# Kernel tuning notes

Measured on AMD Instinct MI355X. Metric: run time of the kernel, lower is better.

The kernel has to match this reference:

```python
import jax, jax.numpy as jnp
import numpy as np


def setup_inputs() -> dict:
    key = jax.random.key(0)
    ks = jax.random.split(key, 8)
    B, H, W = 4, 512, 256
    return {
        "x1": jax.random.normal(ks[0], (B, H, W), dtype=jnp.float32),
        "x2": jax.random.normal(ks[1], (B, H, W), dtype=jnp.float32),
        "wq": jax.random.normal(ks[2], (2, 2), dtype=jnp.float32) * 0.5,
        "bq": jax.random.normal(ks[3], (2,), dtype=jnp.float32) * 0.1,
        "wk": jax.random.normal(ks[4], (2, 2), dtype=jnp.float32) * 0.5,
        "bk": jax.random.normal(ks[5], (2,), dtype=jnp.float32) * 0.1,
        "wv": jax.random.normal(ks[6], (2, 2), dtype=jnp.float32) * 0.5,
        "bv": jax.random.normal(ks[7], (2,), dtype=jnp.float32) * 0.1,
    }


def reference(x1, x2, wq, bq, wk, bk, wv, bv):
    # input: [B, 2, H, W]
    inp = jnp.stack((x1, x2), axis=1)

    def proj(w, b):  # 1x1 conv == channel matmul; -> [B, 2, H, W]
        return jnp.einsum('oi,bihw->bohw', w, inp) + b[None, :, None, None]

    q = proj(wq, bq).transpose(0, 2, 3, 1)  # [B, H, W, 2]
    k = proj(wk, bk).transpose(0, 2, 1, 3)  # [B, H, 2, W]
    v = proj(wv, bv).transpose(0, 2, 3, 1)  # [B, H, W, 2]

    qk = jnp.einsum('bhwc,bhcu->bhwu', q, k)  # [B, H, W, W]
    score = jax.nn.softmax(qk, axis=-1)
    out = jnp.einsum('bhwu,bhuc->bhwc', score, v)  # [B, H, W, 2]

    out1 = x1 + out[..., 0]
    out2 = x2 + out[..., 1]
    return (out1, out2)
```

## Files before the change

kernel.cpp:

```cpp
#include <hip/hip_runtime.h>

typedef float v2f __attribute__((ext_vector_type(2)));

#define LOG2E 1.4426950408889634f

__device__ __forceinline__ float fast_exp2(float x) {
#if __has_builtin(__builtin_amdgcn_exp2f)
    return __builtin_amdgcn_exp2f(x);
#else
    return exp2f(x);
#endif
}

__device__ __forceinline__ v2f pk_fma(v2f a, v2f b, v2f c) {
    return __builtin_elementwise_fma(a, b, c);
}

__global__ __launch_bounds__(256, 2) void csa_kernel(
    const float* __restrict__ x1, const float* __restrict__ x2,
    const float* __restrict__ wq, const float* __restrict__ bq,
    const float* __restrict__ wk, const float* __restrict__ bk,
    const float* __restrict__ wv, const float* __restrict__ bv,
    float* __restrict__ out1, float* __restrict__ out2)
{
    constexpr int W = 256;
    __shared__ float4 sK[4][W / 2];
    __shared__ float4 sV[4][W / 2];

    const int tid = threadIdx.x;
    const int wv_id = tid >> 6;
    const int l = tid & 63;
    const long row = (long)blockIdx.x * 4 + wv_id;
    const long base = row * W;

    const float4 xa = *(const float4*)(x1 + base + 4 * l);
    const float4 xb = *(const float4*)(x2 + base + 4 * l);
    const float X1[4] = {xa.x, xa.y, xa.z, xa.w};
    const float X2[4] = {xb.x, xb.y, xb.z, xb.w};

    const float wq00 = wq[0], wq01 = wq[1], wq10 = wq[2], wq11 = wq[3];
    const float wk00 = wk[0], wk01 = wk[1], wk10 = wk[2], wk11 = wk[3];
    const float wv00 = wv[0], wv01 = wv[1], wv10 = wv[2], wv11 = wv[3];
    const float bq0 = bq[0], bq1 = bq[1];
    const float bk0 = bk[0], bk1 = bk[1];
    const float bv0 = bv[0], bv1 = bv[1];

    float q0[4], q1[4], k0[4], k1[4], v0[4], v1[4];
#pragma unroll
    for (int j = 0; j < 4; ++j) {
        q0[j] = fmaf(wq00, X1[j], fmaf(wq01, X2[j], bq0));
        q1[j] = fmaf(wq10, X1[j], fmaf(wq11, X2[j], bq1));
        k0[j] = fmaf(wk00, X1[j], fmaf(wk01, X2[j], bk0));
        k1[j] = fmaf(wk10, X1[j], fmaf(wk11, X2[j], bk1));
        v0[j] = fmaf(wv00, X1[j], fmaf(wv01, X2[j], bv0));
        v1[j] = fmaf(wv10, X1[j], fmaf(wv11, X2[j], bv1));
    }

    sK[wv_id][2 * l + 0] = make_float4(k0[0], k0[1], k1[0], k1[1]);
    sK[wv_id][2 * l + 1] = make_float4(k0[2], k0[3], k1[2], k1[3]);
    sV[wv_id][2 * l + 0] = make_float4(v0[0], v0[1], v1[0], v1[1]);
    sV[wv_id][2 * l + 1] = make_float4(v0[2], v0[3], v1[2], v1[3]);

    float q2 = 0.f, k2 = 0.f;
#pragma unroll
    for (int j = 0; j < 4; ++j) {
        q2 = fmaxf(q2, fmaf(q0[j], q0[j], q1[j] * q1[j]));
        k2 = fmaxf(k2, fmaf(k0[j], k0[j], k1[j] * k1[j]));
    }
#pragma unroll
    for (int off = 32; off >= 1; off >>= 1) {
        q2 = fmaxf(q2, __shfl_xor(q2, off, 64));
        k2 = fmaxf(k2, __shfl_xor(k2, off, 64));
    }
    const float mb = sqrtf(q2 * k2);
    const float csh = -mb * LOG2E;

    __syncthreads();

    const v2f cshv = {csh, csh};
    v2f ql0[4], ql1[4], sum[4], o0[4], o1[4];
#pragma unroll
    for (int j = 0; j < 4; ++j) {
        const float a0 = q0[j] * LOG2E, a1 = q1[j] * LOG2E;
        ql0[j] = (v2f){a0, a0};
        ql1[j] = (v2f){a1, a1};
        sum[j] = (v2f){0.f, 0.f};
        o0[j]  = (v2f){0.f, 0.f};
        o1[j]  = (v2f){0.f, 0.f};
    }

#pragma unroll 4
    for (int up = 0; up < W / 2; ++up) {
        const float4 K = sK[wv_id][up];
        const float4 V = sV[wv_id][up];
        const v2f kx = {K.x, K.y};
        const v2f kz = {K.z, K.w};
        const v2f vx = {V.x, V.y};
        const v2f vz = {V.z, V.w};
#pragma unroll
        for (int j = 0; j < 4; ++j) {
            v2f s = pk_fma(ql0[j], kx, pk_fma(ql1[j], kz, cshv));
            v2f e;
            e.x = fast_exp2(s.x);
            e.y = fast_exp2(s.y);
            sum[j] += e;
            o0[j] = pk_fma(e, vx, o0[j]);
            o1[j] = pk_fma(e, vz, o1[j]);
        }
    }

    float r1[4], r2[4];
#pragma unroll
    for (int j = 0; j < 4; ++j) {
        const float s = sum[j].x + sum[j].y;
        const float inv = 1.0f / s;
        r1[j] = fmaf(o0[j].x + o0[j].y, inv, X1[j]);
        r2[j] = fmaf(o1[j].x + o1[j].y, inv, X2[j]);
    }
    *(float4*)(out1 + base + 4 * l) = make_float4(r1[0], r1[1], r1[2], r1[3]);
    *(float4*)(out2 + base + 4 * l) = make_float4(r2[0], r2[1], r2[2], r2[3]);
}

extern "C" void kernel_launch(void* const* d_in, const int* in_sizes, int n_in,
                              void* d_out, int out_size, void* d_ws, size_t ws_size,
                              hipStream_t stream) {
    const float* x1 = (const float*)d_in[0];
    const float* x2 = (const float*)d_in[1];
    const float* wq = (const float*)d_in[2];
    const float* bq = (const float*)d_in[3];
    const float* wk = (const float*)d_in[4];
    const float* bk = (const float*)d_in[5];
    const float* wv = (const float*)d_in[6];
    const float* bv = (const float*)d_in[7];

    float* out = (float*)d_out;
    const int BHW = in_sizes[0];
    const int rows = BHW / 256;

    csa_kernel<<<rows / 4, 256, 0, stream>>>(x1, x2, wq, bq, wk, bk, wv, bv,
                                             out, out + BHW);
}
```

Baseline: 91.63 us.

## Split each attention row's key range across four waves with LDS reduction

Instead of one wave processing a whole row, each block now handles one row and its four waves each process a quarter of the key/value positions. Partial softmax sums and weighted outputs are combined through shared memory, and wave 0 writes the result. This quadruples the number of waves launched to improve occupancy and latency hiding on the exp-heavy loop. In exchange it adds an extra barrier, LDS partial-sum traffic and idle waves during the final combine.

```diff
diff --git a/kernel.cpp b/kernel.cpp
--- a/kernel.cpp
+++ b/kernel.cpp
@@ -16,7 +16,7 @@
     return __builtin_elementwise_fma(a, b, c);
 }
 
-__global__ __launch_bounds__(256, 2) void csa_kernel(
+__global__ __launch_bounds__(256, 4) void csa_kernel(
     const float* __restrict__ x1, const float* __restrict__ x2,
     const float* __restrict__ wq, const float* __restrict__ bq,
     const float* __restrict__ wk, const float* __restrict__ bk,
@@ -24,14 +24,16 @@
     float* __restrict__ out1, float* __restrict__ out2)
 {
     constexpr int W = 256;
-    __shared__ float4 sK[4][W / 2];
-    __shared__ float4 sV[4][W / 2];
+    __shared__ float4 sK[W / 2];
+    __shared__ float4 sV[W / 2];
+    __shared__ float4 pS[4][64];
+    __shared__ float4 pA[4][64];
+    __shared__ float4 pB[4][64];
 
     const int tid = threadIdx.x;
-    const int wv_id = tid >> 6;
+    const int wid = tid >> 6;
     const int l = tid & 63;
-    const long row = (long)blockIdx.x * 4 + wv_id;
-    const long base = row * W;
+    const long base = (long)blockIdx.x * W;
 
     const float4 xa = *(const float4*)(x1 + base + 4 * l);
     const float4 xb = *(const float4*)(x2 + base + 4 * l);
@@ -40,26 +42,32 @@
 
     const float wq00 = wq[0], wq01 = wq[1], wq10 = wq[2], wq11 = wq[3];
     const float wk00 = wk[0], wk01 = wk[1], wk10 = wk[2], wk11 = wk[3];
-    const float wv00 = wv[0], wv01 = wv[1], wv10 = wv[2], wv11 = wv[3];
     const float bq0 = bq[0], bq1 = bq[1];
     const float bk0 = bk[0], bk1 = bk[1];
-    const float bv0 = bv[0], bv1 = bv[1];
 
-    float q0[4], q1[4], k0[4], k1[4], v0[4], v1[4];
+    float q0[4], q1[4], k0[4], k1[4];
 #pragma unroll
     for (int j = 0; j < 4; ++j) {
         q0[j] = fmaf(wq00, X1[j], fmaf(wq01, X2[j], bq0));
         q1[j] = fmaf(wq10, X1[j], fmaf(wq11, X2[j], bq1));
         k0[j] = fmaf(wk00, X1[j], fmaf(wk01, X2[j], bk0));
         k1[j] = fmaf(wk10, X1[j], fmaf(wk11, X2[j], bk1));
-        v0[j] = fmaf(wv00, X1[j], fmaf(wv01, X2[j], bv0));
-        v1[j] = fmaf(wv10, X1[j], fmaf(wv11, X2[j], bv1));
     }
 
-    sK[wv_id][2 * l + 0] = make_float4(k0[0], k0[1], k1[0], k1[1]);
-    sK[wv_id][2 * l + 1] = make_float4(k0[2], k0[3], k1[2], k1[3]);
-    sV[wv_id][2 * l + 0] = make_float4(v0[0], v0[1], v1[0], v1[1]);
-    sV[wv_id][2 * l + 1] = make_float4(v0[2], v0[3], v1[2], v1[3]);
+    if (wid == 0) {
+        const float wv00 = wv[0], wv01 = wv[1], wv10 = wv[2], wv11 = wv[3];
+        const float bv0 = bv[0], bv1 = bv[1];
+        float v0[4], v1[4];
+#pragma unroll
+        for (int j = 0; j < 4; ++j) {
+            v0[j] = fmaf(wv00, X1[j], fmaf(wv01, X2[j], bv0));
+            v1[j] = fmaf(wv10, X1[j], fmaf(wv11, X2[j], bv1));
+        }
+        sK[2 * l + 0] = make_float4(k0[0], k0[1], k1[0], k1[1]);
+        sK[2 * l + 1] = make_float4(k0[2], k0[3], k1[2], k1[3]);
+        sV[2 * l + 0] = make_float4(v0[0], v0[1], v1[0], v1[1]);
+        sV[2 * l + 1] = make_float4(v0[2], v0[3], v1[2], v1[3]);
+    }
 
     float q2 = 0.f, k2 = 0.f;
 #pragma unroll
@@ -74,10 +82,8 @@
     }
     const float mb = sqrtf(q2 * k2);
     const float csh = -mb * LOG2E;
+    const v2f cshv = {csh, csh};
 
-    __syncthreads();
-
-    const v2f cshv = {csh, csh};
     v2f ql0[4], ql1[4], sum[4], o0[4], o1[4];
 #pragma unroll
     for (int j = 0; j < 4; ++j) {
@@ -89,10 +95,13 @@
         o1[j]  = (v2f){0.f, 0.f};
     }
 
+    __syncthreads();
+
+    const int up0 = 32 * wid;
 #pragma unroll 4
-    for (int up = 0; up < W / 2; ++up) {
-        const float4 K = sK[wv_id][up];
-        const float4 V = sV[wv_id][up];
+    for (int up = up0; up < up0 + 32; ++up) {
+        const float4 K = sK[up];
+        const float4 V = sV[up];
         const v2f kx = {K.x, K.y};
         const v2f kz = {K.z, K.w};
         const v2f vx = {V.x, V.y};
@@ -109,16 +118,35 @@
         }
     }
 
-    float r1[4], r2[4];
+    pS[wid][l] = make_float4(sum[0].x + sum[0].y, sum[1].x + sum[1].y,
+                             sum[2].x + sum[2].y, sum[3].x + sum[3].y);
+    pA[wid][l] = make_float4(o0[0].x + o0[0].y, o0[1].x + o0[1].y,
+                             o0[2].x + o0[2].y, o0[3].x + o0[3].y);
+    pB[wid][l] = make_float4(o1[0].x + o1[0].y, o1[1].x + o1[1].y,
+                             o1[2].x + o1[2].y, o1[3].x + o1[3].y);
+
+    __syncthreads();
+
+    if (wid == 0) {
+        const float4 s0 = pS[0][l], s1 = pS[1][l], s2 = pS[2][l], s3 = pS[3][l];
+        const float4 a0 = pA[0][l], a1 = pA[1][l], a2 = pA[2][l], a3 = pA[3][l];
+        const float4 b0 = pB[0][l], b1 = pB[1][l], b2 = pB[2][l], b3 = pB[3][l];
+        const float S[4] = {s0.x + s1.x + s2.x + s3.x, s0.y + s1.y + s2.y + s3.y,
+                            s0.z + s1.z + s2.z + s3.z, s0.w + s1.w + s2.w + s3.w};
+        const float A[4] = {a0.x + a1.x + a2.x + a3.x, a0.y + a1.y + a2.y + a3.y,
+                            a0.z + a1.z + a2.z + a3.z, a0.w + a1.w + a2.w + a3.w};
+        const float Bv[4] = {b0.x + b1.x + b2.x + b3.x, b0.y + b1.y + b2.y + b3.y,
+                             b0.z + b1.z + b2.z + b3.z, b0.w + b1.w + b2.w + b3.w};
+        float r1[4], r2[4];
 #pragma unroll
-    for (int j = 0; j < 4; ++j) {
-        const float s = sum[j].x + sum[j].y;
-        const float inv = 1.0f / s;
-        r1[j] = fmaf(o0[j].x + o0[j].y, inv, X1[j]);
-        r2[j] = fmaf(o1[j].x + o1[j].y, inv, X2[j]);
+        for (int j = 0; j < 4; ++j) {
+            const float inv = 1.0f / S[j];
+            r1[j] = fmaf(A[j], inv, X1[j]);
+            r2[j] = fmaf(Bv[j], inv, X2[j]);
+        }
+        *(float4*)(out1 + base + 4 * l) = make_float4(r1[0], r1[1], r1[2], r1[3]);
+        *(float4*)(out2 + base + 4 * l) = make_float4(r2[0], r2[1], r2[2], r2[3]);
     }
-    *(float4*)(out1 + base + 4 * l) = make_float4(r1[0], r1[1], r1[2], r1[3]);
-    *(float4*)(out2 + base + 4 * l) = make_float4(r2[0], r2[1], r2[2], r2[3]);
 }
 
 extern "C" void kernel_launch(void* const* d_in, const int* in_sizes, int n_in,
@@ -137,6 +165,6 @@
     const int BHW = in_sizes[0];
     const int rows = BHW / 256;
 
-    csa_kernel<<<rows / 4, 256, 0, stream>>>(x1, x2, wq, bq, wk, bk, wv, bv,
-                                             out, out + BHW);
+    csa_kernel<<<rows, 256, 0, stream>>>(x1, x2, wq, bq, wk, bk, wv, bv,
+                                         out, out + BHW);
 }
```

Result: faster. 89.82 us (-2.0%).
